# Kernel optimization log

Measured on AMD Instinct MI355X. Metric: run time of the kernel, lower is better.

## Reference

```python
import jax, jax.numpy as jnp
import numpy as np

N_NODES = 50000
N_EDGES = 800000
IN_DIM, HID_DIM, OUT_DIM = 128, 128, 64


def setup_inputs() -> dict:
    key = jax.random.key(0)
    ks = jax.random.split(key, 12)
    x = jax.random.normal(ks[0], (N_NODES, IN_DIM), dtype=jnp.float32)
    src = jax.random.randint(ks[1], (N_EDGES,), 0, N_NODES, dtype=jnp.int32)
    dst = jax.random.randint(ks[2], (N_EDGES,), 0, N_NODES, dtype=jnp.int32)
    def lin(k, fan_in, fan_out):
        s = 1.0 / np.sqrt(fan_in)
        kw, kb = jax.random.split(k)
        W = jax.random.uniform(kw, (fan_in, fan_out), jnp.float32, -s, s)
        b = jax.random.uniform(kb, (fan_out,), jnp.float32, -s, s)
        return W, b
    W1, b1 = lin(ks[3], IN_DIM, HID_DIM)
    W2, b2 = lin(ks[4], HID_DIM, HID_DIM)
    W3, b3 = lin(ks[5], HID_DIM, OUT_DIM)
    Wf, bf = lin(ks[6], OUT_DIM, 1)
    return {"x": x, "src": src, "dst": dst,
            "W1": W1, "b1": b1, "W2": W2, "b2": b2,
            "W3": W3, "b3": b3, "Wf": Wf, "bf": bf}


def reference(x, src, dst, W1, b1, W2, b2, W3, b3, Wf, bf):
    n = x.shape[0]
    # GCN symmetric norm with self-loops: deg = in-degree + 1 (self loop)
    ones = jnp.ones(src.shape[0], x.dtype)
    deg = jax.ops.segment_sum(ones, dst, num_segments=n) + 1.0
    dinv = jax.lax.rsqrt(deg)                       # [N]
    edge_norm = dinv[src] * dinv[dst]               # [E]
    self_norm = dinv * dinv                         # [N], self-loop weight

    def gcn(h, W, b):
        h = h @ W                                   # transform first (PyG order)
        agg = jax.ops.segment_sum(h[src] * edge_norm[:, None], dst, num_segments=n)
        agg = agg + h * self_norm[:, None]          # self-loop contribution
        return agg + b

    h = jax.nn.relu(gcn(x, W1, b1))
    h = jax.nn.relu(gcn(h, W2, b2))
    h = jax.nn.relu(gcn(h, W3, b3))
    return h @ Wf + bf                              # [N, 1] per-node scores
```

## Files before the change

### kernel.cpp

```cpp
#include <hip/hip_runtime.h>
#include <hip/hip_bf16.h>

typedef short bf16x8 __attribute__((ext_vector_type(8)));
typedef float f32x4 __attribute__((ext_vector_type(4)));
typedef _Float16 f16x2 __attribute__((ext_vector_type(2)));

static __device__ __forceinline__ unsigned short f2bf_rne(float f) {
    unsigned int u = __float_as_uint(f);
    u += 0x7fff + ((u >> 16) & 1);
    return (unsigned short)(u >> 16);
}
static __device__ __forceinline__ float bf2f(unsigned short h) {
    return __uint_as_float(((unsigned int)h) << 16);
}

static __device__ __forceinline__ void wsplit_one(const float* W, unsigned short* hi,
                                                  unsigned short* lo, int BN, int idx) {
    int k = idx / BN, n = idx % BN;
    float w = W[idx];
    unsigned short h = f2bf_rne(w);
    unsigned short l = f2bf_rne(w - bf2f(h));
    int CT = BN >> 4;
    int kc = k >> 5, quad = (k >> 3) & 3, j = k & 7;
    int ct = n >> 4, c = n & 15;
    int slot = (((kc * CT + ct) * 4 + quad) * 16 + c) * 8 + j;
    hi[slot] = h;
    lo[slot] = l;
}


template<int BN>
static __device__ __forceinline__ void gemm_body(const float* __restrict__ A,
                        const unsigned short* __restrict__ Whi, const unsigned short* __restrict__ Wlo,
                        _Float16* __restrict__ C, int N, int blk,
                        unsigned short* AhiS, unsigned short* AloS) {
    constexpr int CT = BN / 16;
    const int tid = threadIdx.x;
    const int wave = tid >> 6;
    const int lane = tid & 63;
    const int quad = lane >> 4;
    const int c16 = lane & 15;
    const int row0 = blk * 64;

    f32x4 acc[CT];
    #pragma unroll
    for (int t = 0; t < CT; ++t) acc[t] = (f32x4){0.f, 0.f, 0.f, 0.f};

    for (int kc = 0; kc < 4; ++kc) {
        #pragma unroll
        for (int r = 0; r < 2; ++r) {
            int f4 = tid + r * 256;
            int arow = f4 >> 3;
            int c4 = f4 & 7;
            int grow = row0 + arow;
            float4 v = make_float4(0.f, 0.f, 0.f, 0.f);
            if (grow < N) v = *(const float4*)&A[(size_t)grow * 128 + kc * 32 + c4 * 4];
            unsigned short h0 = f2bf_rne(v.x), h1 = f2bf_rne(v.y), h2 = f2bf_rne(v.z), h3 = f2bf_rne(v.w);
            ushort4 hv = make_ushort4(h0, h1, h2, h3);
            ushort4 lv = make_ushort4(f2bf_rne(v.x - bf2f(h0)), f2bf_rne(v.y - bf2f(h1)),
                                      f2bf_rne(v.z - bf2f(h2)), f2bf_rne(v.w - bf2f(h3)));
            int q = c4 >> 1;
            int joff = (c4 & 1) * 4;
            int base = (q * 64 + arow) * 8 + joff;
            *(ushort4*)&AhiS[base] = hv;
            *(ushort4*)&AloS[base] = lv;
        }
        __syncthreads();

        int abase = (quad * 64 + wave * 16 + c16) * 8;
        bf16x8 ahi = *(const bf16x8*)&AhiS[abase];
        bf16x8 alo = *(const bf16x8*)&AloS[abase];

        #pragma unroll
        for (int ct = 0; ct < CT; ++ct) {
            size_t bslot = ((size_t)(kc * CT + ct) * 64 + lane) * 8;
            bf16x8 bhi = *(const bf16x8*)&Whi[bslot];
            bf16x8 blo = *(const bf16x8*)&Wlo[bslot];
            acc[ct] = __builtin_amdgcn_mfma_f32_16x16x32_bf16(ahi, bhi, acc[ct], 0, 0, 0);
            acc[ct] = __builtin_amdgcn_mfma_f32_16x16x32_bf16(ahi, blo, acc[ct], 0, 0, 0);
            acc[ct] = __builtin_amdgcn_mfma_f32_16x16x32_bf16(alo, bhi, acc[ct], 0, 0, 0);
        }
        __syncthreads();
    }

    #pragma unroll
    for (int ct = 0; ct < CT; ++ct) {
        #pragma unroll
        for (int r = 0; r < 4; ++r) {
            int grow = row0 + wave * 16 + quad * 4 + r;
            if (grow < N) C[(size_t)grow * BN + ct * 16 + c16] = (_Float16)acc[ct][r];
        }
    }
}


__global__ __launch_bounds__(256) void k_count_wsplit(const int* __restrict__ dst, int* __restrict__ deg,
                          int* __restrict__ rank,
                          const float* __restrict__ W1, const float* __restrict__ W2, const float* __restrict__ W3,
                          unsigned short* __restrict__ W1hi, unsigned short* __restrict__ W1lo,
                          unsigned short* __restrict__ W2hi, unsigned short* __restrict__ W2lo,
                          unsigned short* __restrict__ W3hi, unsigned short* __restrict__ W3lo,
                          int E) {
    int e = blockIdx.x * blockDim.x + threadIdx.x;
    if (e < E) rank[e] = atomicAdd(&deg[dst[e]], 1);
    if (e < 128 * 128) {
        wsplit_one(W1, W1hi, W1lo, 128, e);
        wsplit_one(W2, W2hi, W2lo, 128, e);
    }
    if (e < 128 * 64) wsplit_one(W3, W3hi, W3lo, 64, e);
}

__global__ __launch_bounds__(1024) void k_scan(const int* __restrict__ deg, float* __restrict__ dinv,
                                               int* __restrict__ row_start, int N) {
    __shared__ int s[1024];
    __shared__ int wsum[16];
    __shared__ int prefix;
    const int t = threadIdx.x;
    const int base = blockIdx.x * 1024;

    {
        int v = 0;
        for (int j = t; j < base; j += 1024) v += deg[j];
        for (int off = 32; off > 0; off >>= 1) v += __shfl_down(v, off, 64);
        if ((t & 63) == 0) wsum[t >> 6] = v;
        __syncthreads();
        if (t == 0) {
            int acc = 0;
            #pragma unroll
            for (int k = 0; k < 16; ++k) acc += wsum[k];
            prefix = acc;
        }
    }

    int i = base + t;
    int v = 0;
    if (i < N) {
        v = deg[i];
        dinv[i] = rsqrtf((float)v + 1.0f);
    }
    s[t] = v;
    __syncthreads();
    for (int off = 1; off < 1024; off <<= 1) {
        int x = (t >= off) ? s[t - off] : 0;
        __syncthreads();
        s[t] += x;
        __syncthreads();
    }
    if (i <= N) row_start[i] = prefix + s[t] - v;
}


__global__ __launch_bounds__(256, 2) void k_gemm1_scatter(const float* __restrict__ A,
                          const unsigned short* __restrict__ Whi, const unsigned short* __restrict__ Wlo,
                          _Float16* __restrict__ C, int N, int gemmGrid,
                          const int* __restrict__ src, const int* __restrict__ dst,
                          const int* __restrict__ row_start, const int* __restrict__ rank,
                          const float* __restrict__ dinv, int2* __restrict__ cv, int E) {
    __shared__ unsigned short AhiS[4 * 64 * 8];
    __shared__ unsigned short AloS[4 * 64 * 8];
    if ((int)blockIdx.x < gemmGrid) {
        gemm_body<128>(A, Whi, Wlo, C, N, blockIdx.x, AhiS, AloS);
    } else {
        int e = (blockIdx.x - gemmGrid) * 256 + threadIdx.x;
        if (e < E) {
            int d = dst[e];
            int s = src[e];
            cv[row_start[d] + rank[e]] = make_int2(s, __float_as_int(dinv[s]));
        }
    }
}

template<int BN>
__global__ __launch_bounds__(256, 2) void k_gemm_mfma(const float* __restrict__ A,
                        const unsigned short* __restrict__ Whi, const unsigned short* __restrict__ Wlo,
                        _Float16* __restrict__ C, int N) {
    __shared__ unsigned short AhiS[4 * 64 * 8];
    __shared__ unsigned short AloS[4 * 64 * 8];
    gemm_body<BN>(A, Whi, Wlo, C, N, blockIdx.x, AhiS, AloS);
}


__global__ __launch_bounds__(256) void k_agg128(const _Float16* __restrict__ t, float* __restrict__ outp,
                      const int* __restrict__ row_start, const int2* __restrict__ cv,
                      const float* __restrict__ dinv, const float* __restrict__ bias,
                      int N) {
    int gid = blockIdx.x * blockDim.x + threadIdx.x;
    int node = gid >> 6;
    int lane = gid & 63;
    if (node >= N) return;
    int p = row_start[node];
    int end = row_start[node + 1];
    const f16x2* tp = (const f16x2*)t;
    float2 acc[4];
    #pragma unroll
    for (int j = 0; j < 4; ++j) acc[j] = make_float2(0.f, 0.f);

    while (p < end) {
        int idx = p + lane;
        int2 h = (idx < end) ? cv[idx] : make_int2(0, 0);
        int cnt = min(end - p, 64);
        int rounds = (cnt + 15) >> 4;
        for (int r = 0; r < rounds; ++r) {
            int base = r * 16;
            int s[16]; float w[16];
            #pragma unroll
            for (int j = 0; j < 16; ++j) {
                s[j] = __builtin_amdgcn_readlane(h.x, base + j);
                w[j] = __int_as_float(__builtin_amdgcn_readlane(h.y, base + j));
            }
            f16x2 v[16];
            #pragma unroll
            for (int j = 0; j < 16; ++j) v[j] = tp[s[j] * 64 + lane];
            #pragma unroll
            for (int j = 0; j < 16; ++j) {
                acc[j & 3].x += w[j] * (float)v[j].x;
                acc[j & 3].y += w[j] * (float)v[j].y;
            }
        }
        p += 64;
    }
    float di = dinv[node];
    f16x2 sv = tp[node * 64 + lane];
    float2 bv = ((const float2*)bias)[lane];
    float sx = (acc[0].x + acc[1].x) + (acc[2].x + acc[3].x);
    float sy = (acc[0].y + acc[1].y) + (acc[2].y + acc[3].y);
    float2 r;
    r.x = fmaxf(di * sx + di * di * (float)sv.x + bv.x, 0.f);
    r.y = fmaxf(di * sy + di * di * (float)sv.y + bv.y, 0.f);
    ((float2*)outp)[node * 64 + lane] = r;
}

__global__ __launch_bounds__(256) void k_agg64_final(const _Float16* __restrict__ t, float* __restrict__ outp,
                      const int* __restrict__ row_start, const int2* __restrict__ cv,
                      const float* __restrict__ dinv, const float* __restrict__ bias,
                      const float* __restrict__ Wf, const float* __restrict__ bf,
                      int N) {
    int gid = blockIdx.x * blockDim.x + threadIdx.x;
    int node = gid >> 6;
    int lane = gid & 63;
    if (node >= N) return;
    int p = row_start[node];
    int end = row_start[node + 1];
    float acc[4] = {0.f, 0.f, 0.f, 0.f};

    while (p < end) {
        int idx = p + lane;
        int2 h = (idx < end) ? cv[idx] : make_int2(0, 0);
        int cnt = min(end - p, 64);
        int rounds = (cnt + 15) >> 4;
        for (int r = 0; r < rounds; ++r) {
            int base = r * 16;
            int s[16]; float w[16];
            #pragma unroll
            for (int j = 0; j < 16; ++j) {
                s[j] = __builtin_amdgcn_readlane(h.x, base + j);
                w[j] = __int_as_float(__builtin_amdgcn_readlane(h.y, base + j));
            }
            _Float16 v[16];
            #pragma unroll
            for (int j = 0; j < 16; ++j) v[j] = t[s[j] * 64 + lane];
            #pragma unroll
            for (int j = 0; j < 16; ++j) acc[j & 3] += w[j] * (float)v[j];
        }
        p += 64;
    }
    float di = dinv[node];
    float r = di * ((acc[0] + acc[1]) + (acc[2] + acc[3])) + di * di * (float)t[node * 64 + lane] + bias[lane];
    r = fmaxf(r, 0.f);
    float v = r * Wf[lane];
    for (int off = 32; off > 0; off >>= 1) v += __shfl_down(v, off, 64);
    if (lane == 0) outp[node] = v + bf[0];
}


extern "C" void kernel_launch(void* const* d_in, const int* in_sizes, int n_in,
                              void* d_out, int out_size, void* d_ws, size_t ws_size,
                              hipStream_t stream) {
    const float* x  = (const float*)d_in[0];
    const int*   src = (const int*)d_in[1];
    const int*   dst = (const int*)d_in[2];
    const float* W1 = (const float*)d_in[3];
    const float* b1 = (const float*)d_in[4];
    const float* W2 = (const float*)d_in[5];
    const float* b2 = (const float*)d_in[6];
    const float* W3 = (const float*)d_in[7];
    const float* b3 = (const float*)d_in[8];
    const float* Wf = (const float*)d_in[9];
    const float* bf = (const float*)d_in[10];
    float* out = (float*)d_out;

    const int N = 50000;
    const int E = 800000;

    char* ws = (char*)d_ws;
    size_t off = 0;
    auto alloc = [&](size_t bytes) -> void* {
        void* p = (void*)(ws + off);
        off += (bytes + 511) & ~((size_t)511);
        return p;
    };
    int*   deg       = (int*)alloc((size_t)N * 4);
    float* dinv      = (float*)alloc((size_t)N * 4);
    int*   row_start = (int*)alloc((size_t)(N + 1) * 4);
    int*   rank      = (int*)alloc((size_t)E * 4);
    int2*  cv        = (int2*)alloc((size_t)E * 8);
    _Float16* bufT   = (_Float16*)alloc((size_t)N * 128 * 2);
    float* bufH      = (float*)alloc((size_t)N * 128 * 4);
    unsigned short* W1hi = (unsigned short*)alloc(128 * 128 * 2);
    unsigned short* W1lo = (unsigned short*)alloc(128 * 128 * 2);
    unsigned short* W2hi = (unsigned short*)alloc(128 * 128 * 2);
    unsigned short* W2lo = (unsigned short*)alloc(128 * 128 * 2);
    unsigned short* W3hi = (unsigned short*)alloc(128 * 64 * 2);
    unsigned short* W3lo = (unsigned short*)alloc(128 * 64 * 2);

    hipMemsetAsync(deg, 0, (size_t)N * 4, stream);

    k_count_wsplit<<<(E + 255) / 256, 256, 0, stream>>>(dst, deg, rank, W1, W2, W3,
                                                        W1hi, W1lo, W2hi, W2lo, W3hi, W3lo, E);
    int NB = (N + 1023) / 1024;
    k_scan<<<NB, 1024, 0, stream>>>(deg, dinv, row_start, N);

    int gemmGrid = (N + 63) / 64;
    int scatGrid = (E + 255) / 256;
    int aggGrid = (N * 64 + 255) / 256;

    k_gemm1_scatter<<<gemmGrid + scatGrid, 256, 0, stream>>>(x, W1hi, W1lo, bufT, N, gemmGrid,
                                                             src, dst, row_start, rank, dinv, cv, E);
    k_agg128<<<aggGrid, 256, 0, stream>>>(bufT, bufH, row_start, cv, dinv, b1, N);
    k_gemm_mfma<128><<<gemmGrid, 256, 0, stream>>>(bufH, W2hi, W2lo, bufT, N);
    k_agg128<<<aggGrid, 256, 0, stream>>>(bufT, bufH, row_start, cv, dinv, b2, N);
    k_gemm_mfma<64><<<gemmGrid, 256, 0, stream>>>(bufH, W3hi, W3lo, bufT, N);
    k_agg64_final<<<aggGrid, 256, 0, stream>>>(bufT, out, row_start, cv, dinv, b3, Wf, bf, N);
}
```

Measured before the change: 275.8 us.

## Partition feature matrix into 32-column slabs and aggregate slab-wise with 4 edges per wave

The GEMM output is now stored as column slabs of 32 halves per node. Each aggregation wave handles one slab of one node, with four 16-lane groups processing different edges in parallel and then reducing across groups. The idea is to improve L2 locality of the random gathers by keeping one slab resident, and to raise memory-level parallelism. The cost is that each edge list is read once per slab, the final reduction goes through atomicAdd into an output pre-filled with the bias, and the block-count constant 12500 is hardcoded to N=50000.

```diff
diff --git a/kernel.cpp b/kernel.cpp
--- a/kernel.cpp
+++ b/kernel.cpp
@@ -85,10 +85,12 @@
 
     #pragma unroll
     for (int ct = 0; ct < CT; ++ct) {
+        int col = ct * 16 + c16;
+        _Float16* Cq = C + (size_t)(col >> 5) * N * 32 + (col & 31);
         #pragma unroll
         for (int r = 0; r < 4; ++r) {
             int grow = row0 + wave * 16 + quad * 4 + r;
-            if (grow < N) C[(size_t)grow * BN + ct * 16 + c16] = (_Float16)acc[ct][r];
+            if (grow < N) Cq[(size_t)grow * 32] = (_Float16)acc[ct][r];
         }
     }
 }
@@ -111,7 +113,9 @@
 }
 
 __global__ __launch_bounds__(1024) void k_scan(const int* __restrict__ deg, float* __restrict__ dinv,
-                                               int* __restrict__ row_start, int N) {
+                                               int* __restrict__ row_start,
+                                               float* __restrict__ outp, const float* __restrict__ bf,
+                                               int N) {
     __shared__ int s[1024];
     __shared__ int wsum[16];
     __shared__ int prefix;
@@ -137,6 +141,7 @@
     if (i < N) {
         v = deg[i];
         dinv[i] = rsqrtf((float)v + 1.0f);
+        outp[i] = bf[0];
     }
     s[t] = v;
     __syncthreads();
@@ -180,20 +185,20 @@
 }
 
 
-__global__ __launch_bounds__(256) void k_agg128(const _Float16* __restrict__ t, float* __restrict__ outp,
+__global__ __launch_bounds__(256) void k_agg128q(const _Float16* __restrict__ t, float* __restrict__ outp,
                       const int* __restrict__ row_start, const int2* __restrict__ cv,
                       const float* __restrict__ dinv, const float* __restrict__ bias,
                       int N) {
-    int gid = blockIdx.x * blockDim.x + threadIdx.x;
-    int node = gid >> 6;
-    int lane = gid & 63;
-    if (node >= N) return;
+    int q = blockIdx.x / 12500;
+    int node = (blockIdx.x - q * 12500) * 4 + (threadIdx.x >> 6);
+    int lane = threadIdx.x & 63;
+    int l16 = lane & 15;
+    int g4 = lane >> 4;
+    const f16x2* tp = (const f16x2*)(t + (size_t)q * N * 32);
     int p = row_start[node];
     int end = row_start[node + 1];
-    const f16x2* tp = (const f16x2*)t;
-    float2 acc[4];
-    #pragma unroll
-    for (int j = 0; j < 4; ++j) acc[j] = make_float2(0.f, 0.f);
+    float2 accA = make_float2(0.f, 0.f);
+    float2 accB = make_float2(0.f, 0.f);
 
     while (p < end) {
         int idx = p + lane;
@@ -201,47 +206,53 @@
         int cnt = min(end - p, 64);
         int rounds = (cnt + 15) >> 4;
         for (int r = 0; r < rounds; ++r) {
-            int base = r * 16;
-            int s[16]; float w[16];
-            #pragma unroll
-            for (int j = 0; j < 16; ++j) {
-                s[j] = __builtin_amdgcn_readlane(h.x, base + j);
-                w[j] = __int_as_float(__builtin_amdgcn_readlane(h.y, base + j));
-            }
-            f16x2 v[16];
-            #pragma unroll
-            for (int j = 0; j < 16; ++j) v[j] = tp[s[j] * 64 + lane];
-            #pragma unroll
-            for (int j = 0; j < 16; ++j) {
-                acc[j & 3].x += w[j] * (float)v[j].x;
-                acc[j & 3].y += w[j] * (float)v[j].y;
-            }
+            int base = r * 16 + g4 * 4;
+            int s0 = __shfl(h.x, base + 0, 64), s1 = __shfl(h.x, base + 1, 64);
+            int s2 = __shfl(h.x, base + 2, 64), s3 = __shfl(h.x, base + 3, 64);
+            float w0 = __int_as_float(__shfl(h.y, base + 0, 64));
+            float w1 = __int_as_float(__shfl(h.y, base + 1, 64));
+            float w2 = __int_as_float(__shfl(h.y, base + 2, 64));
+            float w3 = __int_as_float(__shfl(h.y, base + 3, 64));
+            f16x2 v0 = tp[s0 * 16 + l16];
+            f16x2 v1 = tp[s1 * 16 + l16];
+            f16x2 v2 = tp[s2 * 16 + l16];
+            f16x2 v3 = tp[s3 * 16 + l16];
+            accA.x += w0 * (float)v0.x; accA.y += w0 * (float)v0.y;
+            accB.x += w1 * (float)v1.x; accB.y += w1 * (float)v1.y;
+            accA.x += w2 * (float)v2.x; accA.y += w2 * (float)v2.y;
+            accB.x += w3 * (float)v3.x; accB.y += w3 * (float)v3.y;
         }
         p += 64;
     }
+    float sx = accA.x + accB.x;
+    float sy = accA.y + accB.y;
+    sx += __shfl_xor(sx, 16, 64); sx += __shfl_xor(sx, 32, 64);
+    sy += __shfl_xor(sy, 16, 64); sy += __shfl_xor(sy, 32, 64);
+
     float di = dinv[node];
-    f16x2 sv = tp[node * 64 + lane];
-    float2 bv = ((const float2*)bias)[lane];
-    float sx = (acc[0].x + acc[1].x) + (acc[2].x + acc[3].x);
-    float sy = (acc[0].y + acc[1].y) + (acc[2].y + acc[3].y);
-    float2 r;
-    r.x = fmaxf(di * sx + di * di * (float)sv.x + bv.x, 0.f);
-    r.y = fmaxf(di * sy + di * di * (float)sv.y + bv.y, 0.f);
-    ((float2*)outp)[node * 64 + lane] = r;
+    f16x2 sv = tp[node * 16 + l16];
+    float2 bv = ((const float2*)bias)[q * 16 + l16];
+    float rx = fmaxf(di * sx + di * di * (float)sv.x + bv.x, 0.f);
+    float ry = fmaxf(di * sy + di * di * (float)sv.y + bv.y, 0.f);
+    if (lane < 16)
+        ((float2*)outp)[(size_t)node * 64 + q * 16 + l16] = make_float2(rx, ry);
 }
 
 __global__ __launch_bounds__(256) void k_agg64_final(const _Float16* __restrict__ t, float* __restrict__ outp,
                       const int* __restrict__ row_start, const int2* __restrict__ cv,
                       const float* __restrict__ dinv, const float* __restrict__ bias,
-                      const float* __restrict__ Wf, const float* __restrict__ bf,
+                      const float* __restrict__ Wf,
                       int N) {
-    int gid = blockIdx.x * blockDim.x + threadIdx.x;
-    int node = gid >> 6;
-    int lane = gid & 63;
-    if (node >= N) return;
+    int q = blockIdx.x / 12500;
+    int node = (blockIdx.x - q * 12500) * 4 + (threadIdx.x >> 6);
+    int lane = threadIdx.x & 63;
+    int l16 = lane & 15;
+    int g4 = lane >> 4;
+    const f16x2* tp = (const f16x2*)(t + (size_t)q * N * 32);
     int p = row_start[node];
     int end = row_start[node + 1];
-    float acc[4] = {0.f, 0.f, 0.f, 0.f};
+    float2 accA = make_float2(0.f, 0.f);
+    float2 accB = make_float2(0.f, 0.f);
 
     while (p < end) {
         int idx = p + lane;
@@ -249,27 +260,41 @@
         int cnt = min(end - p, 64);
         int rounds = (cnt + 15) >> 4;
         for (int r = 0; r < rounds; ++r) {
-            int base = r * 16;
-            int s[16]; float w[16];
-            #pragma unroll
-            for (int j = 0; j < 16; ++j) {
-                s[j] = __builtin_amdgcn_readlane(h.x, base + j);
-                w[j] = __int_as_float(__builtin_amdgcn_readlane(h.y, base + j));
-            }
-            _Float16 v[16];
-            #pragma unroll
-            for (int j = 0; j < 16; ++j) v[j] = t[s[j] * 64 + lane];
-            #pragma unroll
-            for (int j = 0; j < 16; ++j) acc[j & 3] += w[j] * (float)v[j];
+            int base = r * 16 + g4 * 4;
+            int s0 = __shfl(h.x, base + 0, 64), s1 = __shfl(h.x, base + 1, 64);
+            int s2 = __shfl(h.x, base + 2, 64), s3 = __shfl(h.x, base + 3, 64);
+            float w0 = __int_as_float(__shfl(h.y, base + 0, 64));
+            float w1 = __int_as_float(__shfl(h.y, base + 1, 64));
+            float w2 = __int_as_float(__shfl(h.y, base + 2, 64));
+            float w3 = __int_as_float(__shfl(h.y, base + 3, 64));
+            f16x2 v0 = tp[s0 * 16 + l16];
+            f16x2 v1 = tp[s1 * 16 + l16];
+            f16x2 v2 = tp[s2 * 16 + l16];
+            f16x2 v3 = tp[s3 * 16 + l16];
+            accA.x += w0 * (float)v0.x; accA.y += w0 * (float)v0.y;
+            accB.x += w1 * (float)v1.x; accB.y += w1 * (float)v1.y;
+            accA.x += w2 * (float)v2.x; accA.y += w2 * (float)v2.y;
+            accB.x += w3 * (float)v3.x; accB.y += w3 * (float)v3.y;
         }
         p += 64;
     }
+    float sx = accA.x + accB.x;
+    float sy = accA.y + accB.y;
+    sx += __shfl_xor(sx, 16, 64); sx += __shfl_xor(sx, 32, 64);
+    sy += __shfl_xor(sy, 16, 64); sy += __shfl_xor(sy, 32, 64);
+
     float di = dinv[node];
-    float r = di * ((acc[0] + acc[1]) + (acc[2] + acc[3])) + di * di * (float)t[node * 64 + lane] + bias[lane];
-    r = fmaxf(r, 0.f);
-    float v = r * Wf[lane];
-    for (int off = 32; off > 0; off >>= 1) v += __shfl_down(v, off, 64);
-    if (lane == 0) outp[node] = v + bf[0];
+    f16x2 sv = tp[node * 16 + l16];
+    float2 bv = ((const float2*)bias)[q * 16 + l16];
+    float rx = fmaxf(di * sx + di * di * (float)sv.x + bv.x, 0.f);
+    float ry = fmaxf(di * sy + di * di * (float)sv.y + bv.y, 0.f);
+    float2 wf = ((const float2*)Wf)[q * 16 + l16];
+    float partial = rx * wf.x + ry * wf.y;
+    partial += __shfl_xor(partial, 1, 64);
+    partial += __shfl_xor(partial, 2, 64);
+    partial += __shfl_xor(partial, 4, 64);
+    partial += __shfl_xor(partial, 8, 64);
+    if (lane == 0) atomicAdd(&outp[node], partial);
 }
 
 
@@ -318,17 +343,18 @@
     k_count_wsplit<<<(E + 255) / 256, 256, 0, stream>>>(dst, deg, rank, W1, W2, W3,
                                                         W1hi, W1lo, W2hi, W2lo, W3hi, W3lo, E);
     int NB = (N + 1023) / 1024;
-    k_scan<<<NB, 1024, 0, stream>>>(deg, dinv, row_start, N);
+    k_scan<<<NB, 1024, 0, stream>>>(deg, dinv, row_start, out, bf, N);
 
     int gemmGrid = (N + 63) / 64;
     int scatGrid = (E + 255) / 256;
-    int aggGrid = (N * 64 + 255) / 256;
+    int agg128Grid = N;
+    int agg64Grid  = N / 2;
 
     k_gemm1_scatter<<<gemmGrid + scatGrid, 256, 0, stream>>>(x, W1hi, W1lo, bufT, N, gemmGrid,
                                                              src, dst, row_start, rank, dinv, cv, E);
-    k_agg128<<<aggGrid, 256, 0, stream>>>(bufT, bufH, row_start, cv, dinv, b1, N);
+    k_agg128q<<<agg128Grid, 256, 0, stream>>>(bufT, bufH, row_start, cv, dinv, b1, N);
     k_gemm_mfma<128><<<gemmGrid, 256, 0, stream>>>(bufH, W2hi, W2lo, bufT, N);
-    k_agg128<<<aggGrid, 256, 0, stream>>>(bufT, bufH, row_start, cv, dinv, b2, N);
+    k_agg128q<<<agg128Grid, 256, 0, stream>>>(bufT, bufH, row_start, cv, dinv, b2, N);
     k_gemm_mfma<64><<<gemmGrid, 256, 0, stream>>>(bufH, W3hi, W3lo, bufT, N);
-    k_agg64_final<<<aggGrid, 256, 0, stream>>>(bufT, out, row_start, cv, dinv, b3, Wf, bf, N);
-}
+    k_agg64_final<<<agg64Grid, 256, 0, stream>>>(bufT, out, row_start, cv, dinv, b3, Wf, N);
+}
```

Result: slower. 338.6 us (+22.8%).
